# Kernel optimization log

Hardware: AMD Instinct MI355X
Metric: run time of the kernel (lower is better)

The kernel has to match this reference:

```python
import jax, jax.numpy as jnp
import numpy as np

USER, ITEM, LAYER = 100000, 50000, 3
DIM, NNZ = 64, 6400000


def setup_inputs() -> dict:
    key = jax.random.key(0)
    k1, k2, k3, k4 = jax.random.split(key, 4)
    rows = jax.random.randint(k1, (NNZ,), 0, USER, dtype=jnp.int32)
    cols = jax.random.randint(k2, (NNZ,), 0, ITEM, dtype=jnp.int32)
    vals = jax.random.uniform(k3, (NNZ,), dtype=jnp.float32)
    embeds = jax.random.normal(k4, (USER + ITEM, DIM), dtype=jnp.float32)
    return {"rows": rows, "cols": cols, "vals": vals, "embeds": embeds}


def reference(rows, cols, vals, embeds):
    # LightGCN bipartite propagation: adj is sparse [USER, ITEM] in COO form.
    lats = [embeds]
    gcn_lats = [embeds]
    for _ in range(LAYER):
        user_part = lats[-1][:USER]          # [USER, DIM]
        item_part = lats[-1][USER:]          # [ITEM, DIM]
        # user_embeds = adj @ item_part : scatter-add weighted gathered item rows
        user_embeds = jax.ops.segment_sum(vals[:, None] * item_part[cols], rows,
                                          num_segments=USER)
        # item_embeds = adj.T @ user_part
        item_embeds = jax.ops.segment_sum(vals[:, None] * user_part[rows], cols,
                                          num_segments=ITEM)
        embedding = jnp.concatenate([user_embeds, item_embeds], axis=0)
        gcn_lats.append(embedding)
        lats.append(embedding + lats[-1])    # residual accumulation
    # stack the python lists into arrays: [LAYER+1, USER+ITEM, DIM] each
    return (jnp.stack(lats), jnp.stack(gcn_lats))
```

## Files before the change

### kernel.cpp

```cpp
#include <hip/hip_runtime.h>

#define N_USER 100000
#define N_ITEM 50000
#define N_NODES 150000
#define DIM 64
#define N_NNZ 6400000
#define N_LAYER 3
#define TOTAL_EDGES (2 * N_NNZ)

#define SB_SHIFT 8
#define NODES_PER_SB 256
#define NSB ((N_NODES + NODES_PER_SB - 1) / NODES_PER_SB)
#define NB 256
#define EPB (N_NNZ / NB)
#define BIN_THREADS 1024

__global__ __launch_bounds__(BIN_THREADS) void count_kernel(
    const int* __restrict__ rows,
    const int* __restrict__ cols,
    int* __restrict__ counts)
{
    __shared__ int cnt[NSB];
    for (int i = threadIdx.x; i < NSB; i += BIN_THREADS) cnt[i] = 0;
    __syncthreads();

    const int e0 = blockIdx.x * EPB;
    for (int e = e0 + (int)threadIdx.x; e < e0 + EPB; e += BIN_THREADS) {
        const int r = rows[e];
        const int c = N_USER + cols[e];
        atomicAdd(&cnt[r >> SB_SHIFT], 1);
        atomicAdd(&cnt[c >> SB_SHIFT], 1);
    }
    __syncthreads();

    for (int i = threadIdx.x; i < NSB; i += BIN_THREADS)
        counts[i * NB + blockIdx.x] = cnt[i];
    if (blockIdx.x == 0 && threadIdx.x == 0) counts[NSB * NB] = 0;
}

__global__ __launch_bounds__(1024) void scan_kernel(int* __restrict__ data, int n)
{
    __shared__ int wsum[16];
    __shared__ int woff[16];
    __shared__ int carry_s;
    if (threadIdx.x == 0) carry_s = 0;
    __syncthreads();

    const int lane = threadIdx.x & 63;
    const int wid  = threadIdx.x >> 6;

    for (int base = 0; base < n; base += 1024) {
        int i = base + (int)threadIdx.x;
        int v = (i < n) ? data[i] : 0;

        int incl = v;
        #pragma unroll
        for (int off = 1; off < 64; off <<= 1) {
            int t = __shfl_up(incl, off, 64);
            if (lane >= off) incl += t;
        }
        if (lane == 63) wsum[wid] = incl;
        __syncthreads();

        if (threadIdx.x == 0) {
            int s = carry_s;
            #pragma unroll
            for (int w = 0; w < 16; ++w) { woff[w] = s; s += wsum[w]; }
            carry_s = s;
        }
        __syncthreads();

        if (i < n) data[i] = woff[wid] + incl - v;
        __syncthreads();
    }
}

__global__ __launch_bounds__(BIN_THREADS) void bin2_kernel(
    const int* __restrict__ rows,
    const int* __restrict__ cols,
    const float* __restrict__ vals,
    const int* __restrict__ base,
    int2* __restrict__ binned)
{
    __shared__ int cur[NSB];
    for (int i = threadIdx.x; i < NSB; i += BIN_THREADS)
        cur[i] = base[i * NB + blockIdx.x];
    __syncthreads();

    const int e0 = blockIdx.x * EPB;
    for (int e = e0 + (int)threadIdx.x; e < e0 + EPB; e += BIN_THREADS) {
        const int r  = rows[e];
        const int c  = N_USER + cols[e];
        const int vb = __float_as_int(vals[e]);
        int p1 = atomicAdd(&cur[r >> SB_SHIFT], 1);
        binned[p1] = make_int2(((r & (NODES_PER_SB - 1)) << 18) | c, vb);
        int p2 = atomicAdd(&cur[c >> SB_SHIFT], 1);
        binned[p2] = make_int2(((c & (NODES_PER_SB - 1)) << 18) | r, vb);
    }
}

__global__ __launch_bounds__(1024) void fine_scatter_kernel(
    const int* __restrict__ base,
    const int2* __restrict__ binned,
    int* __restrict__ offsets,
    int2* __restrict__ edges)
{
    const int b   = blockIdx.x;
    const int tid = threadIdx.x;
    const int s0  = base[b * NB];
    const int s1  = base[(b + 1) * NB];

    __shared__ int cnt[NODES_PER_SB];
    __shared__ int ofs[NODES_PER_SB];
    if (tid < NODES_PER_SB) cnt[tid] = 0;
    __syncthreads();

    for (int i = s0 + tid; i < s1; i += 1024)
        atomicAdd(&cnt[binned[i].x >> 18], 1);
    __syncthreads();

    if (tid == 0) {
        int s = 0;
        #pragma unroll 8
        for (int j = 0; j < NODES_PER_SB; ++j) { ofs[j] = s; s += cnt[j]; }
    }
    __syncthreads();

    if (tid < NODES_PER_SB) {
        const int node = b * NODES_PER_SB + tid;
        if (node < N_NODES) offsets[node] = s0 + ofs[tid];
        cnt[tid] = ofs[tid];
    }
    if (b == (int)gridDim.x - 1 && tid == 0) offsets[N_NODES] = TOTAL_EDGES;
    __syncthreads();

    for (int i = s0 + tid; i < s1; i += 1024) {
        int2 rec = binned[i];
        int nl   = rec.x >> 18;
        int src  = rec.x & 0x3FFFF;
        int p    = s0 + atomicAdd(&cnt[nl], 1);
        edges[p] = make_int2(src, rec.y);
    }
}

__global__ __launch_bounds__(256) void gather_kernel(
    const int* __restrict__ offsets,
    const int2* __restrict__ edges,
    const float* __restrict__ lat_prev,
    float* __restrict__ gcn_l,
    float* __restrict__ lat_l)
{
    const int gtid = blockIdx.x * blockDim.x + threadIdx.x;
    const int node = gtid >> 6;
    const int lane = gtid & 63;
    if (node >= N_NODES) return;

    const int beg = offsets[node];
    const int end = offsets[node + 1];
    const long long* ep = reinterpret_cast<const long long*>(edges);

    float acc = 0.f;
    for (int t = beg; t < end; t += 64) {
        const int idx = t + lane;
        long long my = (idx < end) ? __builtin_nontemporal_load(ep + idx) : 0LL;
        const int m = min(64, end - t);
        int k = 0;
        for (; k + 8 <= m; k += 8) {
            long long p0 = __shfl(my, k + 0);
            long long p1 = __shfl(my, k + 1);
            long long p2 = __shfl(my, k + 2);
            long long p3 = __shfl(my, k + 3);
            long long p4 = __shfl(my, k + 4);
            long long p5 = __shfl(my, k + 5);
            long long p6 = __shfl(my, k + 6);
            long long p7 = __shfl(my, k + 7);
            float x0 = lat_prev[(((int)p0) << 6) | lane];
            float x1 = lat_prev[(((int)p1) << 6) | lane];
            float x2 = lat_prev[(((int)p2) << 6) | lane];
            float x3 = lat_prev[(((int)p3) << 6) | lane];
            float x4 = lat_prev[(((int)p4) << 6) | lane];
            float x5 = lat_prev[(((int)p5) << 6) | lane];
            float x6 = lat_prev[(((int)p6) << 6) | lane];
            float x7 = lat_prev[(((int)p7) << 6) | lane];
            acc += __int_as_float((int)(p0 >> 32)) * x0;
            acc += __int_as_float((int)(p1 >> 32)) * x1;
            acc += __int_as_float((int)(p2 >> 32)) * x2;
            acc += __int_as_float((int)(p3 >> 32)) * x3;
            acc += __int_as_float((int)(p4 >> 32)) * x4;
            acc += __int_as_float((int)(p5 >> 32)) * x5;
            acc += __int_as_float((int)(p6 >> 32)) * x6;
            acc += __int_as_float((int)(p7 >> 32)) * x7;
        }
        for (; k < m; ++k) {
            long long p = __shfl(my, k);
            acc += __int_as_float((int)(p >> 32)) * lat_prev[(((int)p) << 6) | lane];
        }
    }

    const int o = gtid;
    __builtin_nontemporal_store(acc, &gcn_l[o]);
    __builtin_nontemporal_store(lat_prev[o] + acc, &lat_l[o]);
}

__global__ __launch_bounds__(256) void histogram_kernel(
    const int* __restrict__ rows,
    const int* __restrict__ cols,
    int* __restrict__ counts)
{
    int e = blockIdx.x * blockDim.x + threadIdx.x;
    if (e >= N_NNZ) return;
    atomicAdd(&counts[rows[e]], 1);
    atomicAdd(&counts[N_USER + cols[e]], 1);
}

__global__ __launch_bounds__(256) void fill_kernel(
    const int* __restrict__ rows,
    const int* __restrict__ cols,
    const float* __restrict__ vals,
    int* __restrict__ cursor,
    int2* __restrict__ edges)
{
    int e = blockIdx.x * blockDim.x + threadIdx.x;
    if (e >= N_NNZ) return;
    const int r = rows[e];
    const int c = cols[e];
    const int vb = __float_as_int(vals[e]);
    int pu = atomicAdd(&cursor[r], 1);
    edges[pu] = make_int2(N_USER + c, vb);
    int pi = atomicAdd(&cursor[N_USER + c], 1);
    edges[pi] = make_int2(r, vb);
}

__global__ __launch_bounds__(256) void scatter_kernel(
    const int* __restrict__ rows,
    const int* __restrict__ cols,
    const float* __restrict__ vals,
    const float* __restrict__ lat_prev,
    float* __restrict__ gcn_out)
{
    const int gtid = blockIdx.x * blockDim.x + threadIdx.x;
    const int edge = gtid >> 6;
    const int lane = gtid & 63;
    if (edge >= N_NNZ) return;
    const int r = rows[edge];
    const int c = cols[edge];
    const float v = vals[edge];
    atomicAdd(&gcn_out[(size_t)r * DIM + lane],
              v * lat_prev[(size_t)(N_USER + c) * DIM + lane]);
    atomicAdd(&gcn_out[(size_t)(N_USER + c) * DIM + lane],
              v * lat_prev[(size_t)r * DIM + lane]);
}

__global__ __launch_bounds__(256) void residual_add_kernel(
    const float4* __restrict__ a,
    const float4* __restrict__ b,
    float4* __restrict__ out,
    int n4)
{
    int i = blockIdx.x * blockDim.x + threadIdx.x;
    if (i < n4) {
        float4 av = a[i], bv = b[i];
        out[i] = make_float4(av.x + bv.x, av.y + bv.y, av.z + bv.z, av.w + bv.w);
    }
}

extern "C" void kernel_launch(void* const* d_in, const int* in_sizes, int n_in,
                              void* d_out, int out_size, void* d_ws, size_t ws_size,
                              hipStream_t stream) {
    const int*   rows   = (const int*)d_in[0];
    const int*   cols   = (const int*)d_in[1];
    const float* vals   = (const float*)d_in[2];
    const float* embeds = (const float*)d_in[3];

    float* out = (float*)d_out;
    const size_t N = (size_t)N_NODES * DIM;

    float* lats = out;
    float* gcn  = out + 4 * N;

    hipMemcpyAsync(lats, embeds, N * sizeof(float), hipMemcpyDeviceToDevice, stream);
    hipMemcpyAsync(gcn,  embeds, N * sizeof(float), hipMemcpyDeviceToDevice, stream);

    const size_t edges_bytes = (size_t)TOTAL_EDGES * sizeof(int2);

    const size_t mat_bytes   = (size_t)(NSB * NB + 1) * sizeof(int);
    const size_t offs_off    = (mat_bytes + 15) & ~(size_t)15;
    const size_t offs_bytes  = (size_t)(N_NODES + 1) * sizeof(int);
    const size_t binned_off  = (offs_off + offs_bytes + 15) & ~(size_t)15;
    const size_t edges2_off  = (binned_off + edges_bytes + 15) & ~(size_t)15;
    const size_t need_sort   = edges2_off + edges_bytes;

    const size_t t2_off_bytes    = (size_t)(N_NODES + 1) * sizeof(int);
    const size_t t2_cursor_off   = (t2_off_bytes + 15) & ~(size_t)15;
    const size_t t2_cursor_bytes = (size_t)N_NODES * sizeof(int);
    const size_t t2_edges_off    = (t2_cursor_off + t2_cursor_bytes + 15) & ~(size_t)15;
    const size_t need_old        = t2_edges_off + edges_bytes;

    const int eb = (N_NNZ + 255) / 256;
    const int gb = (N_NODES * 64 + 255) / 256;

    if (ws_size >= need_sort) {
        int*  mat     = (int*)d_ws;
        int*  offsets = (int*)((char*)d_ws + offs_off);
        int2* binned  = (int2*)((char*)d_ws + binned_off);
        int2* edges   = (int2*)((char*)d_ws + edges2_off);

        count_kernel<<<NB, BIN_THREADS, 0, stream>>>(rows, cols, mat);
        scan_kernel<<<1, 1024, 0, stream>>>(mat, NSB * NB + 1);
        bin2_kernel<<<NB, BIN_THREADS, 0, stream>>>(rows, cols, vals, mat, binned);
        fine_scatter_kernel<<<NSB, 1024, 0, stream>>>(mat, binned, offsets, edges);

        for (int l = 1; l <= N_LAYER; ++l) {
            const float* lat_prev = lats + (size_t)(l - 1) * N;
            gather_kernel<<<gb, 256, 0, stream>>>(
                offsets, edges, lat_prev,
                gcn  + (size_t)l * N,
                lats + (size_t)l * N);
        }
    } else if (ws_size >= need_old) {
        int*  offsets = (int*)d_ws;
        int*  cursor  = (int*)((char*)d_ws + t2_cursor_off);
        int2* edges   = (int2*)((char*)d_ws + t2_edges_off);

        hipMemsetAsync(offsets, 0, t2_off_bytes, stream);
        histogram_kernel<<<eb, 256, 0, stream>>>(rows, cols, offsets);
        scan_kernel<<<1, 1024, 0, stream>>>(offsets, N_NODES + 1);
        hipMemcpyAsync(cursor, offsets, t2_cursor_bytes, hipMemcpyDeviceToDevice, stream);
        fill_kernel<<<eb, 256, 0, stream>>>(rows, cols, vals, cursor, edges);

        for (int l = 1; l <= N_LAYER; ++l) {
            const float* lat_prev = lats + (size_t)(l - 1) * N;
            gather_kernel<<<gb, 256, 0, stream>>>(
                offsets, edges, lat_prev,
                gcn  + (size_t)l * N,
                lats + (size_t)l * N);
        }
    } else {
        hipMemsetAsync(gcn + N, 0, 3 * N * sizeof(float), stream);
        const int scatter_blocks = (N_NNZ * 64 + 255) / 256;
        const int n4 = (int)(N / 4);
        const int add_blocks = (n4 + 255) / 256;
        for (int l = 1; l <= N_LAYER; ++l) {
            const float* lat_prev = lats + (size_t)(l - 1) * N;
            float* gcn_l = gcn  + (size_t)l * N;
            float* lat_l = lats + (size_t)l * N;
            scatter_kernel<<<scatter_blocks, 256, 0, stream>>>(
                rows, cols, vals, lat_prev, gcn_l);
            residual_add_kernel<<<add_blocks, 256, 0, stream>>>(
                (const float4*)lat_prev, (const float4*)gcn_l, (float4*)lat_l, n4);
        }
    }
}
```

Measured before the change: 1.848 ms.

## Parallelize bucket scan, sub-sort edges by source, and unroll gather by 16

Three separate changes. The single-block serial scan over the bucket-count matrix becomes a three-kernel multi-block scan (local tile scan, scan of tile totals, add-back). The fine scatter now keys each edge by destination node plus a coarse source bucket, so the edges of a node are grouped by source range and the gathered rows are read with better locality. The gather loop gains a 16-way unrolled path for more loads in flight, at the cost of more registers and possibly lower occupancy.

```diff
diff --git a/kernel.cpp b/kernel.cpp
--- a/kernel.cpp
+++ b/kernel.cpp
@@ -15,6 +15,14 @@
 #define EPB (N_NNZ / NB)
 #define BIN_THREADS 1024
 
+#define SRC_BK_SHIFT 14
+#define NBK 10
+#define NKEY (NODES_PER_SB * NBK)
+
+#define SCAN_N (NSB * NB + 1)
+#define SCAN_TILE 4096
+#define NSCAN ((SCAN_N + SCAN_TILE - 1) / SCAN_TILE)
+
 __global__ __launch_bounds__(BIN_THREADS) void count_kernel(
     const int* __restrict__ rows,
     const int* __restrict__ cols,
@@ -38,40 +46,84 @@
     if (blockIdx.x == 0 && threadIdx.x == 0) counts[NSB * NB] = 0;
 }
 
-__global__ __launch_bounds__(1024) void scan_kernel(int* __restrict__ data, int n)
+__global__ __launch_bounds__(1024) void scan_local_kernel(
+    int* __restrict__ data, int n, int* __restrict__ totals)
 {
     __shared__ int wsum[16];
     __shared__ int woff[16];
-    __shared__ int carry_s;
-    if (threadIdx.x == 0) carry_s = 0;
-    __syncthreads();
-
-    const int lane = threadIdx.x & 63;
-    const int wid  = threadIdx.x >> 6;
-
-    for (int base = 0; base < n; base += 1024) {
-        int i = base + (int)threadIdx.x;
-        int v = (i < n) ? data[i] : 0;
-
-        int incl = v;
+    const int tid  = threadIdx.x;
+    const int lane = tid & 63;
+    const int wid  = tid >> 6;
+    const int idx  = blockIdx.x * SCAN_TILE + tid * 4;
+
+    int v0 = 0, v1 = 0, v2 = 0, v3 = 0;
+    if (idx + 3 < n) {
+        int4 t = *reinterpret_cast<const int4*>(data + idx);
+        v0 = t.x; v1 = t.y; v2 = t.z; v3 = t.w;
+    } else {
+        if (idx     < n) v0 = data[idx];
+        if (idx + 1 < n) v1 = data[idx + 1];
+        if (idx + 2 < n) v2 = data[idx + 2];
+        if (idx + 3 < n) v3 = data[idx + 3];
+    }
+    const int tsum = v0 + v1 + v2 + v3;
+
+    int incl = tsum;
+    #pragma unroll
+    for (int off = 1; off < 64; off <<= 1) {
+        int t = __shfl_up(incl, off, 64);
+        if (lane >= off) incl += t;
+    }
+    if (lane == 63) wsum[wid] = incl;
+    __syncthreads();
+
+    if (tid == 0) {
+        int s = 0;
         #pragma unroll
-        for (int off = 1; off < 64; off <<= 1) {
-            int t = __shfl_up(incl, off, 64);
-            if (lane >= off) incl += t;
-        }
-        if (lane == 63) wsum[wid] = incl;
-        __syncthreads();
-
-        if (threadIdx.x == 0) {
-            int s = carry_s;
-            #pragma unroll
-            for (int w = 0; w < 16; ++w) { woff[w] = s; s += wsum[w]; }
-            carry_s = s;
-        }
-        __syncthreads();
-
-        if (i < n) data[i] = woff[wid] + incl - v;
-        __syncthreads();
+        for (int w = 0; w < 16; ++w) { woff[w] = s; s += wsum[w]; }
+        totals[blockIdx.x] = s;
+    }
+    __syncthreads();
+
+    const int e0 = woff[wid] + incl - tsum;
+    const int e1 = e0 + v0;
+    const int e2 = e1 + v1;
+    const int e3 = e2 + v2;
+    if (idx + 3 < n) {
+        *reinterpret_cast<int4*>(data + idx) = make_int4(e0, e1, e2, e3);
+    } else {
+        if (idx     < n) data[idx]     = e0;
+        if (idx + 1 < n) data[idx + 1] = e1;
+        if (idx + 2 < n) data[idx + 2] = e2;
+        if (idx + 3 < n) data[idx + 3] = e3;
+    }
+}
+
+__global__ __launch_bounds__(64) void scan_totals_kernel(int* __restrict__ totals, int n)
+{
+    const int lane = threadIdx.x;
+    int v = (lane < n) ? totals[lane] : 0;
+    int incl = v;
+    #pragma unroll
+    for (int off = 1; off < 64; off <<= 1) {
+        int t = __shfl_up(incl, off, 64);
+        if (lane >= off) incl += t;
+    }
+    if (lane < n) totals[lane] = incl - v;
+}
+
+__global__ __launch_bounds__(256) void scan_add_kernel(
+    int* __restrict__ data, int n, const int* __restrict__ totals)
+{
+    const int idx = (blockIdx.x * 256 + threadIdx.x) * 4;
+    if (idx >= n) return;
+    const int add = totals[idx >> 12];
+    if (idx + 3 < n) {
+        int4 t = *reinterpret_cast<const int4*>(data + idx);
+        *reinterpret_cast<int4*>(data + idx) =
+            make_int4(t.x + add, t.y + add, t.z + add, t.w + add);
+    } else {
+        for (int j = 0; j < 4 && idx + j < n; ++j) data[idx + j] += add;
     }
 }
 
@@ -110,35 +162,51 @@
     const int s0  = base[b * NB];
     const int s1  = base[(b + 1) * NB];
 
-    __shared__ int cnt[NODES_PER_SB];
-    __shared__ int ofs[NODES_PER_SB];
-    if (tid < NODES_PER_SB) cnt[tid] = 0;
-    __syncthreads();
-
-    for (int i = s0 + tid; i < s1; i += 1024)
-        atomicAdd(&cnt[binned[i].x >> 18], 1);
-    __syncthreads();
-
-    if (tid == 0) {
+    __shared__ int cnt[NKEY];
+    __shared__ int ofs[NKEY];
+    for (int k = tid; k < NKEY; k += 1024) cnt[k] = 0;
+    __syncthreads();
+
+    for (int i = s0 + tid; i < s1; i += 1024) {
+        const int x   = binned[i].x;
+        const int key = (x >> 18) * NBK + ((x & 0x3FFFF) >> SRC_BK_SHIFT);
+        atomicAdd(&cnt[key], 1);
+    }
+    __syncthreads();
+
+    if (tid < 64) {
         int s = 0;
-        #pragma unroll 8
-        for (int j = 0; j < NODES_PER_SB; ++j) { ofs[j] = s; s += cnt[j]; }
+        for (int j = 0; j < NKEY / 64; ++j) s += cnt[tid * (NKEY / 64) + j];
+        int incl = s;
+        #pragma unroll
+        for (int off = 1; off < 64; off <<= 1) {
+            int t = __shfl_up(incl, off, 64);
+            if (tid >= off) incl += t;
+        }
+        int run = incl - s;
+        for (int j = 0; j < NKEY / 64; ++j) {
+            const int k = tid * (NKEY / 64) + j;
+            const int v = cnt[k];
+            ofs[k] = run;
+            run += v;
+        }
     }
     __syncthreads();
 
     if (tid < NODES_PER_SB) {
         const int node = b * NODES_PER_SB + tid;
-        if (node < N_NODES) offsets[node] = s0 + ofs[tid];
-        cnt[tid] = ofs[tid];
+        if (node < N_NODES) offsets[node] = s0 + ofs[tid * NBK];
     }
     if (b == (int)gridDim.x - 1 && tid == 0) offsets[N_NODES] = TOTAL_EDGES;
+
+    for (int k = tid; k < NKEY; k += 1024) cnt[k] = ofs[k];
     __syncthreads();
 
     for (int i = s0 + tid; i < s1; i += 1024) {
         int2 rec = binned[i];
-        int nl   = rec.x >> 18;
-        int src  = rec.x & 0x3FFFF;
-        int p    = s0 + atomicAdd(&cnt[nl], 1);
+        const int src = rec.x & 0x3FFFF;
+        const int key = (rec.x >> 18) * NBK + (src >> SRC_BK_SHIFT);
+        const int p   = s0 + atomicAdd(&cnt[key], 1);
         edges[p] = make_int2(src, rec.y);
     }
 }
@@ -165,6 +233,56 @@
         long long my = (idx < end) ? __builtin_nontemporal_load(ep + idx) : 0LL;
         const int m = min(64, end - t);
         int k = 0;
+        for (; k + 16 <= m; k += 16) {
+            long long p0  = __shfl(my, k + 0);
+            long long p1  = __shfl(my, k + 1);
+            long long p2  = __shfl(my, k + 2);
+            long long p3  = __shfl(my, k + 3);
+            long long p4  = __shfl(my, k + 4);
+            long long p5  = __shfl(my, k + 5);
+            long long p6  = __shfl(my, k + 6);
+            long long p7  = __shfl(my, k + 7);
+            long long p8  = __shfl(my, k + 8);
+            long long p9  = __shfl(my, k + 9);
+            long long p10 = __shfl(my, k + 10);
+            long long p11 = __shfl(my, k + 11);
+            long long p12 = __shfl(my, k + 12);
+            long long p13 = __shfl(my, k + 13);
+            long long p14 = __shfl(my, k + 14);
+            long long p15 = __shfl(my, k + 15);
+            float x0  = lat_prev[(((int)p0)  << 6) | lane];
+            float x1  = lat_prev[(((int)p1)  << 6) | lane];
+            float x2  = lat_prev[(((int)p2)  << 6) | lane];
+            float x3  = lat_prev[(((int)p3)  << 6) | lane];
+            float x4  = lat_prev[(((int)p4)  << 6) | lane];
+            float x5  = lat_prev[(((int)p5)  << 6) | lane];
+            float x6  = lat_prev[(((int)p6)  << 6) | lane];
+            float x7  = lat_prev[(((int)p7)  << 6) | lane];
+            float x8  = lat_prev[(((int)p8)  << 6) | lane];
+            float x9  = lat_prev[(((int)p9)  << 6) | lane];
+            float x10 = lat_prev[(((int)p10) << 6) | lane];
+            float x11 = lat_prev[(((int)p11) << 6) | lane];
+            float x12 = lat_prev[(((int)p12) << 6) | lane];
+            float x13 = lat_prev[(((int)p13) << 6) | lane];
+            float x14 = lat_prev[(((int)p14) << 6) | lane];
+            float x15 = lat_prev[(((int)p15) << 6) | lane];
+            acc += __int_as_float((int)(p0  >> 32)) * x0;
+            acc += __int_as_float((int)(p1  >> 32)) * x1;
+            acc += __int_as_float((int)(p2  >> 32)) * x2;
+            acc += __int_as_float((int)(p3  >> 32)) * x3;
+            acc += __int_as_float((int)(p4  >> 32)) * x4;
+            acc += __int_as_float((int)(p5  >> 32)) * x5;
+            acc += __int_as_float((int)(p6  >> 32)) * x6;
+            acc += __int_as_float((int)(p7  >> 32)) * x7;
+            acc += __int_as_float((int)(p8  >> 32)) * x8;
+            acc += __int_as_float((int)(p9  >> 32)) * x9;
+            acc += __int_as_float((int)(p10 >> 32)) * x10;
+            acc += __int_as_float((int)(p11 >> 32)) * x11;
+            acc += __int_as_float((int)(p12 >> 32)) * x12;
+            acc += __int_as_float((int)(p13 >> 32)) * x13;
+            acc += __int_as_float((int)(p14 >> 32)) * x14;
+            acc += __int_as_float((int)(p15 >> 32)) * x15;
+        }
         for (; k + 8 <= m; k += 8) {
             long long p0 = __shfl(my, k + 0);
             long long p1 = __shfl(my, k + 1);
@@ -213,6 +331,43 @@
     atomicAdd(&counts[N_USER + cols[e]], 1);
 }
 
+__global__ __launch_bounds__(1024) void scan_kernel(int* __restrict__ data, int n)
+{
+    __shared__ int wsum[16];
+    __shared__ int woff[16];
+    __shared__ int carry_s;
+    if (threadIdx.x == 0) carry_s = 0;
+    __syncthreads();
+
+    const int lane = threadIdx.x & 63;
+    const int wid  = threadIdx.x >> 6;
+
+    for (int base = 0; base < n; base += 1024) {
+        int i = base + (int)threadIdx.x;
+        int v = (i < n) ? data[i] : 0;
+
+        int incl = v;
+        #pragma unroll
+        for (int off = 1; off < 64; off <<= 1) {
+            int t = __shfl_up(incl, off, 64);
+            if (lane >= off) incl += t;
+        }
+        if (lane == 63) wsum[wid] = incl;
+        __syncthreads();
+
+        if (threadIdx.x == 0) {
+            int s = carry_s;
+            #pragma unroll
+            for (int w = 0; w < 16; ++w) { woff[w] = s; s += wsum[w]; }
+            carry_s = s;
+        }
+        __syncthreads();
+
+        if (i < n) data[i] = woff[wid] + incl - v;
+        __syncthreads();
+    }
+}
+
 __global__ __launch_bounds__(256) void fill_kernel(
     const int* __restrict__ rows,
     const int* __restrict__ cols,
@@ -283,10 +438,12 @@
 
     const size_t edges_bytes = (size_t)TOTAL_EDGES * sizeof(int2);
 
-    const size_t mat_bytes   = (size_t)(NSB * NB + 1) * sizeof(int);
+    const size_t mat_bytes   = (size_t)SCAN_N * sizeof(int);
     const size_t offs_off    = (mat_bytes + 15) & ~(size_t)15;
     const size_t offs_bytes  = (size_t)(N_NODES + 1) * sizeof(int);
-    const size_t binned_off  = (offs_off + offs_bytes + 15) & ~(size_t)15;
+    const size_t tot_off     = (offs_off + offs_bytes + 15) & ~(size_t)15;
+    const size_t tot_bytes   = (size_t)NSCAN * sizeof(int);
+    const size_t binned_off  = (tot_off + tot_bytes + 15) & ~(size_t)15;
     const size_t edges2_off  = (binned_off + edges_bytes + 15) & ~(size_t)15;
     const size_t need_sort   = edges2_off + edges_bytes;
 
@@ -302,11 +459,14 @@
     if (ws_size >= need_sort) {
         int*  mat     = (int*)d_ws;
         int*  offsets = (int*)((char*)d_ws + offs_off);
+        int*  totals  = (int*)((char*)d_ws + tot_off);
         int2* binned  = (int2*)((char*)d_ws + binned_off);
         int2* edges   = (int2*)((char*)d_ws + edges2_off);
 
         count_kernel<<<NB, BIN_THREADS, 0, stream>>>(rows, cols, mat);
-        scan_kernel<<<1, 1024, 0, stream>>>(mat, NSB * NB + 1);
+        scan_local_kernel<<<NSCAN, 1024, 0, stream>>>(mat, SCAN_N, totals);
+        scan_totals_kernel<<<1, 64, 0, stream>>>(totals, NSCAN);
+        scan_add_kernel<<<(SCAN_N + 1023) / 1024, 256, 0, stream>>>(mat, SCAN_N, totals);
         bin2_kernel<<<NB, BIN_THREADS, 0, stream>>>(rows, cols, vals, mat, binned);
         fine_scatter_kernel<<<NSB, 1024, 0, stream>>>(mat, binned, offsets, edges);
 
```

After: 1.770 ms. 1.04x faster.
